# Performance work log

Hardware: AMD Instinct MI355X
Metric: run time of the kernel (lower is better)

## Reference

```python
import jax, jax.numpy as jnp
import numpy as np

B, S, D = 1, 2048, 4096
H, KV, HD = 32, 8, 128
REP = H // KV


def setup_inputs() -> dict:
    key = jax.random.key(0)
    ks = jax.random.split(key, 8)
    x = jax.random.normal(ks[0], (B, S, D), dtype=jnp.float32)
    # RoPE tables: freqs_cis[s, j] = exp(i * s * theta_j), theta_j = 10000^(-2j/HD)
    inv_freq = 1.0 / (10000.0 ** (jnp.arange(0, HD, 2, dtype=jnp.float32) / HD))  # [HD/2]
    ang = jnp.arange(S, dtype=jnp.float32)[:, None] * inv_freq[None, :]          # [S, HD/2]
    freqs_cos, freqs_sin = jnp.cos(ang), jnp.sin(ang)
    # causal additive mask [S, S]
    mask = jnp.where(jnp.tril(jnp.ones((S, S), dtype=bool)), 0.0, -1e9).astype(jnp.float32)
    scale = 0.02
    wq = jax.random.normal(ks[1], (D, H * HD), dtype=jnp.float32) * scale
    wk = jax.random.normal(ks[2], (D, KV * HD), dtype=jnp.float32) * scale
    wv = jax.random.normal(ks[3], (D, KV * HD), dtype=jnp.float32) * scale
    wo = jax.random.normal(ks[4], (H * HD, D), dtype=jnp.float32) * scale
    return {"x": x, "freqs_cos": freqs_cos, "freqs_sin": freqs_sin, "mask": mask,
            "wq": wq, "wk": wk, "wv": wv, "wo": wo, "start_pos": 0}


def _rope(t, cos, sin):
    # t: [B, S, nH, HD]; cos/sin: [S, HD/2]. Complex mult on interleaved pairs.
    b, s, h, hd = t.shape
    tp = t.reshape(b, s, h, hd // 2, 2)
    a, bb = tp[..., 0], tp[..., 1]
    c = cos[None, :, None, :]
    sn = sin[None, :, None, :]
    out = jnp.stack([a * c - bb * sn, a * sn + bb * c], axis=-1)
    return out.reshape(b, s, h, hd)


def reference(x, freqs_cos, freqs_sin, mask, wq, wk, wv, wo, start_pos):
    bsz, seqlen, _ = x.shape
    xq = (x @ wq).reshape(bsz, seqlen, H, HD)
    xk = (x @ wk).reshape(bsz, seqlen, KV, HD)
    xv = (x @ wv).reshape(bsz, seqlen, KV, HD)
    xq = _rope(xq, freqs_cos, freqs_sin)
    xk = _rope(xk, freqs_cos, freqs_sin)
    # start_pos == 0: cache = current xk/xv. GQA: group queries by kv head
    # instead of duplicating K/V (same math as repeat_kv).
    q = xq.reshape(bsz, seqlen, KV, REP, HD)
    scores = jnp.einsum('bqkrd,bskd->bkrqs', q, xk) / np.sqrt(HD).astype(np.float32)
    scores = scores + mask[None, None, None, :, :]
    probs = jax.nn.softmax(scores.astype(jnp.float32), axis=-1).astype(x.dtype)
    out = jnp.einsum('bkrqs,bskd->bqkrd', probs, xv)
    out = out.reshape(bsz, seqlen, H * HD)
    return out @ wo
```

## Files before the change

kernel.cpp:

```cpp
#include <hip/hip_runtime.h>

typedef unsigned short u16;
typedef unsigned int u32;
typedef unsigned long long u64;

typedef float f32x4 __attribute__((ext_vector_type(4)));
typedef __bf16 bf16x8 __attribute__((ext_vector_type(8)));
typedef u16 u16x4 __attribute__((ext_vector_type(4)));
typedef u16 u16x8 __attribute__((ext_vector_type(8)));
typedef float fx4 __attribute__((ext_vector_type(4)));


static __device__ __forceinline__ u16 f2b(float f) {
  u32 u = __builtin_bit_cast(u32, f);
  return (u16)((u + 0x7fffu + ((u >> 16) & 1u)) >> 16);
}
static __device__ __forceinline__ float b2f(u16 b) {
  return __builtin_bit_cast(float, ((u32)b) << 16);
}
static __device__ __forceinline__ void gload_lds16(const void* g, void* l) {
  auto gp = (const __attribute__((address_space(1))) u32*)(u64)g;
  auto lp = (__attribute__((address_space(3))) u32*)(u32)(u64)l;
  __builtin_amdgcn_global_load_lds(gp, lp, 16, 0, 0);
}

__global__ __launch_bounds__(256) void cast_bf16_kernel(const float* __restrict__ in,
                                                        u16* __restrict__ out) {
  size_t i = (size_t)(blockIdx.x * 256 + threadIdx.x) * 4;
  fx4 v = *(const fx4*)(in + i);
  u16x4 o;
  o[0] = f2b(v[0]); o[1] = f2b(v[1]); o[2] = f2b(v[2]); o[3] = f2b(v[3]);
  *(u16x4*)(out + i) = o;
}

__global__ __launch_bounds__(256) void wtrans_kernel(const float* __restrict__ in,
                                                     u16* __restrict__ out, int K, int N) {
  __shared__ float tile[32][33];
  int n0 = blockIdx.x * 32, k0 = blockIdx.y * 32;
  int t = threadIdx.x;
  int r = t >> 3, c4 = (t & 7) * 4;
  fx4 v = *(const fx4*)(in + (size_t)(k0 + r) * N + n0 + c4);
  tile[r][c4 + 0] = v[0]; tile[r][c4 + 1] = v[1];
  tile[r][c4 + 2] = v[2]; tile[r][c4 + 3] = v[3];
  __syncthreads();
  u16x4 o;
  o[0] = f2b(tile[c4 + 0][r]); o[1] = f2b(tile[c4 + 1][r]);
  o[2] = f2b(tile[c4 + 2][r]); o[3] = f2b(tile[c4 + 3][r]);
  *(u16x4*)(out + (size_t)(n0 + r) * K + k0 + c4) = o;
}

template <int NH, int LD>
__global__ __launch_bounds__(256) void rope_kernel(u16* __restrict__ x,
                                                   const float* __restrict__ cosb,
                                                   const float* __restrict__ sinb) {
  int tid = blockIdx.x * 256 + threadIdx.x;
  int s = tid / (NH * 16);
  int rem = tid % (NH * 16);
  int h = rem >> 4, c = rem & 15;
  u16* p = x + (size_t)s * LD + h * 128 + c * 8;
  u16x8 v = *(const u16x8*)p;
  fx4 cs = *(const fx4*)(cosb + s * 64 + c * 4);
  fx4 sn = *(const fx4*)(sinb + s * 64 + c * 4);
  u16x8 o;
#pragma unroll
  for (int j = 0; j < 4; ++j) {
    float a = b2f(v[2 * j]), b = b2f(v[2 * j + 1]);
    o[2 * j]     = f2b(a * cs[j] - b * sn[j]);
    o[2 * j + 1] = f2b(a * sn[j] + b * cs[j]);
  }
  *(u16x8*)p = o;
}

__global__ __launch_bounds__(256) void vtrans_kernel(const u16* __restrict__ vb,
                                                     u16* __restrict__ vT) {
  __shared__ u16 tile[64][72];
  int s0 = blockIdx.x * 64;
  int d0 = blockIdx.y * 64;
  int h  = blockIdx.z;
  int t = threadIdx.x;
#pragma unroll
  for (int it = 0; it < 2; ++it) {
    int lin = it * 2048 + t * 8;
    int r = lin >> 6, c = lin & 63;
    u16x8 v = *(const u16x8*)(vb + (size_t)(s0 + r) * 6144 + h * 128 + d0 + c);
#pragma unroll
    for (int j = 0; j < 8; ++j) tile[r][c + j] = v[j];
  }
  __syncthreads();
#pragma unroll
  for (int it = 0; it < 2; ++it) {
    int lin = it * 2048 + t * 8;
    int dd = lin >> 6, ss = lin & 63;
    u16x8 o;
#pragma unroll
    for (int j = 0; j < 8; ++j) o[j] = tile[ss + j][dd];
    *(u16x8*)(vT + (size_t)h * 262144 + (size_t)(d0 + dd) * 2048 + s0 + ss) = o;
  }
}

template <int OUT_BF16>
__global__ __launch_bounds__(256) void gemm_bt_kernel(const u16* __restrict__ A,
                                                      const u16* __restrict__ Bt,
                                                      void* __restrict__ Cv,
                                                      int M, int N, int K) {
  __shared__ u16 sA[128 * 64];
  __shared__ u16 sB[128 * 64];
  const int tid = threadIdx.x;
  const int lane = tid & 63;
  const int w = tid >> 6;
  const int wr = w >> 1, wc = w & 1;
  const int l15 = lane & 15, l4 = lane >> 4;
  const int cpx = gridDim.x >> 3;
  const int swz = ((int)blockIdx.x & 7) * cpx + ((int)blockIdx.x >> 3);
  const int m0 = (swz & 15) * 128;
  const int n0 = (swz >> 4) * 128;

  f32x4 acc[4][4] = {};

  for (int kt = 0; kt < K; kt += 64) {
#pragma unroll
    for (int it = 0; it < 4; ++it) {
      int off = it * 4096 + tid * 16;
      int row = off >> 7;
      int c = ((off >> 4) & 7) ^ (row & 7);
      gload_lds16(A + (size_t)(m0 + row) * K + kt + c * 8, (char*)sA + off);
      gload_lds16(Bt + (size_t)(n0 + row) * K + kt + c * 8, (char*)sB + off);
    }
    __syncthreads();
#pragma unroll
    for (int ks = 0; ks < 2; ++ks) {
      bf16x8 av[4], bv[4];
#pragma unroll
      for (int i = 0; i < 4; ++i) {
        int arow = wr * 64 + i * 16 + l15;
        av[i] = *(const bf16x8*)((char*)sA + arow * 128 + (((ks * 4 + l4) ^ (arow & 7)) << 4));
        int brow = wc * 64 + i * 16 + l15;
        bv[i] = *(const bf16x8*)((char*)sB + brow * 128 + (((ks * 4 + l4) ^ (brow & 7)) << 4));
      }
#pragma unroll
      for (int i = 0; i < 4; ++i)
#pragma unroll
        for (int j = 0; j < 4; ++j)
          acc[i][j] = __builtin_amdgcn_mfma_f32_16x16x32_bf16(av[i], bv[j], acc[i][j], 0, 0, 0);
    }
    __syncthreads();
  }

#pragma unroll
  for (int i = 0; i < 4; ++i)
#pragma unroll
    for (int j = 0; j < 4; ++j) {
      int col = n0 + wc * 64 + j * 16 + l15;
#pragma unroll
      for (int r = 0; r < 4; ++r) {
        int row = m0 + wr * 64 + i * 16 + l4 * 4 + r;
        if (OUT_BF16) ((u16*)Cv)[(size_t)row * N + col] = f2b(acc[i][j][r]);
        else          ((float*)Cv)[(size_t)row * N + col] = acc[i][j][r];
      }
    }
}

__global__ __launch_bounds__(256) void attn_kernel(const u16* __restrict__ qkv,
                                                   const u16* __restrict__ vT,
                                                   u16* __restrict__ ob) {
  __shared__ u16 sK[2][64 * 128];
  __shared__ u16 sV[2][64 * 128];
  __shared__ u16 sP[4][32 * 64];
  const int tid = threadIdx.x, lane = tid & 63, w = tid >> 6;
  const int l15 = lane & 15, l4 = lane >> 4;
  const int h = blockIdx.x;
  const int t = 15 - (int)blockIdx.y;
  const int kvh = h >> 2;
  const int q0 = t * 128;
  const int nt = 2 * t + 2;
  const float scale = 0.08838834764831845f;

  const u16* qb = qkv;
  const u16* kb = qkv + 4096;

  bf16x8 aq[2][4];
#pragma unroll
  for (int m = 0; m < 2; ++m)
#pragma unroll
    for (int kc = 0; kc < 4; ++kc)
      aq[m][kc] = *(const bf16x8*)(qb + (size_t)(q0 + w * 32 + m * 16 + l15) * 6144 +
                                   h * 128 + kc * 32 + l4 * 8);

  f32x4 o[2][8] = {};
  float mrun[2][4], lrun[2][4];
#pragma unroll
  for (int m = 0; m < 2; ++m)
#pragma unroll
    for (int i = 0; i < 4; ++i) { mrun[m][i] = -1e30f; lrun[m][i] = 0.f; }

  auto STAGE = [&](int b, int tt) {
    int s0 = tt * 64;
#pragma unroll
    for (int it = 0; it < 4; ++it) {
      int off = it * 4096 + tid * 16;
      int row = off >> 8;
      int c = ((off >> 4) & 15) ^ (row & 15);
      gload_lds16(kb + (size_t)(s0 + row) * 6144 + kvh * 128 + c * 8, (char*)sK[b] + off);
    }
#pragma unroll
    for (int it = 0; it < 4; ++it) {
      int off = it * 4096 + tid * 16;
      int row = off >> 7;
      int c = ((off >> 4) & 7) ^ (row & 7);
      gload_lds16(vT + (size_t)kvh * 262144 + (size_t)row * 2048 + s0 + c * 8,
                  (char*)sV[b] + off);
    }
  };

  STAGE(0, 0);
  __syncthreads();
  int cur = 0;

  for (int tt = 0; tt < nt; ++tt) {
    if (tt + 1 < nt) STAGE(cur ^ 1, tt + 1);
    int s0 = tt * 64;
    u16* wp = &sP[w][0];

#pragma unroll
    for (int m = 0; m < 2; ++m) {
      const int frow0 = q0 + w * 32 + m * 16;
      if (s0 > frow0 + 15) continue;
      const bool has_mask = (s0 + 63 > frow0);

      f32x4 sf[4] = {};
#pragma unroll
      for (int kc = 0; kc < 4; ++kc) {
#pragma unroll
        for (int j = 0; j < 4; ++j) {
          int krow = j * 16 + l15;
          bf16x8 bk = *(const bf16x8*)((char*)sK[cur] + krow * 256 +
                                       (((kc * 4 + l4) ^ (krow & 15)) << 4));
          sf[j] = __builtin_amdgcn_mfma_f32_16x16x32_bf16(aq[m][kc], bk, sf[j], 0, 0, 0);
        }
      }

      float pv[4][4], mloc[4], lsum[4];
#pragma unroll
      for (int i = 0; i < 4; ++i) mloc[i] = -1e30f;
#pragma unroll
      for (int j = 0; j < 4; ++j) {
        int col = s0 + j * 16 + l15;
#pragma unroll
        for (int i = 0; i < 4; ++i) {
          float v = sf[j][i] * scale;
          if (has_mask && col > frow0 + l4 * 4 + i) v = -1e9f;
          pv[j][i] = v;
          mloc[i] = fmaxf(mloc[i], v);
        }
      }
#pragma unroll
      for (int off = 1; off < 16; off <<= 1)
#pragma unroll
        for (int i = 0; i < 4; ++i) mloc[i] = fmaxf(mloc[i], __shfl_xor(mloc[i], off, 64));
      float alpha[4];
#pragma unroll
      for (int i = 0; i < 4; ++i) {
        float mn = fmaxf(mrun[m][i], mloc[i]);
        alpha[i] = __expf(mrun[m][i] - mn);
        mrun[m][i] = mn;
        lsum[i] = 0.f;
      }
#pragma unroll
      for (int j = 0; j < 4; ++j)
#pragma unroll
        for (int i = 0; i < 4; ++i) {
          float p = __expf(pv[j][i] - mrun[m][i]);
          pv[j][i] = p;
          lsum[i] += p;
        }
#pragma unroll
      for (int off = 1; off < 16; off <<= 1)
#pragma unroll
        for (int i = 0; i < 4; ++i) lsum[i] += __shfl_xor(lsum[i], off, 64);
#pragma unroll
      for (int i = 0; i < 4; ++i) lrun[m][i] = lrun[m][i] * alpha[i] + lsum[i];
#pragma unroll
      for (int n = 0; n < 8; ++n)
#pragma unroll
        for (int i = 0; i < 4; ++i) o[m][n][i] *= alpha[i];

#pragma unroll
      for (int j = 0; j < 4; ++j)
#pragma unroll
        for (int i = 0; i < 4; ++i) {
          int r = m * 16 + l4 * 4 + i;
          int colb = (j * 16 + l15) * 2;
          *(u16*)((char*)wp + r * 128 + (colb ^ ((r & 7) << 4))) = f2b(pv[j][i]);
        }
#pragma unroll
      for (int ks = 0; ks < 2; ++ks) {
        int prow = m * 16 + l15;
        int pb = (ks * 32 + l4 * 8) * 2;
        bf16x8 pa = *(const bf16x8*)((char*)wp + prow * 128 + (pb ^ ((prow & 7) << 4)));
#pragma unroll
        for (int n = 0; n < 8; ++n) {
          int vrow = n * 16 + l15;
          bf16x8 vv = *(const bf16x8*)((char*)sV[cur] + vrow * 128 +
                                       (((ks * 4 + l4) ^ (vrow & 7)) << 4));
          o[m][n] = __builtin_amdgcn_mfma_f32_16x16x32_bf16(pa, vv, o[m][n], 0, 0, 0);
        }
      }
    }
    __syncthreads();
    cur ^= 1;
  }

#pragma unroll
  for (int m = 0; m < 2; ++m) {
    float rcp[4];
#pragma unroll
    for (int i = 0; i < 4; ++i) rcp[i] = 1.f / lrun[m][i];
#pragma unroll
    for (int n = 0; n < 8; ++n)
#pragma unroll
      for (int i = 0; i < 4; ++i) {
        int row = q0 + w * 32 + m * 16 + l4 * 4 + i;
        int col = h * 128 + n * 16 + l15;
        ob[(size_t)row * 4096 + col] = f2b(o[m][n][i] * rcp[i]);
      }
  }
}

extern "C" void kernel_launch(void* const* d_in, const int* in_sizes, int n_in,
                              void* d_out, int out_size, void* d_ws, size_t ws_size,
                              hipStream_t stream) {
  const float* x  = (const float*)d_in[0];
  const float* fc = (const float*)d_in[1];
  const float* fs = (const float*)d_in[2];
  const float* wq = (const float*)d_in[4];
  const float* wk = (const float*)d_in[5];
  const float* wv = (const float*)d_in[6];
  const float* wo = (const float*)d_in[7];
  float* out = (float*)d_out;
  char* ws = (char*)d_ws;

  u16* xb   = (u16*)(ws + 0);
  u16* qkv  = (u16*)(ws + 16777216);
  u16* ob   = (u16*)(ws + 41943040);
  u16* wT   = (u16*)(ws + 58720256);
  u16* vT   = (u16*)(ws + 109051904);
  u16* woT  = wT;

  cast_bf16_kernel<<<8192, 256, 0, stream>>>(x, xb);
  wtrans_kernel<<<dim3(128, 128), 256, 0, stream>>>(wq, wT, 4096, 4096);
  wtrans_kernel<<<dim3(32, 128), 256, 0, stream>>>(wk, wT + (size_t)4096 * 4096, 4096, 1024);
  wtrans_kernel<<<dim3(32, 128), 256, 0, stream>>>(wv, wT + (size_t)5120 * 4096, 4096, 1024);

  gemm_bt_kernel<1><<<768, 256, 0, stream>>>(xb, wT, qkv, 2048, 6144, 4096);

  rope_kernel<32, 6144><<<4096, 256, 0, stream>>>(qkv, fc, fs);
  rope_kernel<8, 6144><<<1024, 256, 0, stream>>>(qkv + 4096, fc, fs);
  vtrans_kernel<<<dim3(32, 2, 8), 256, 0, stream>>>(qkv + 5120, vT);

  attn_kernel<<<dim3(32, 16), 256, 0, stream>>>(qkv, vT, ob);

  wtrans_kernel<<<dim3(128, 128), 256, 0, stream>>>(wo, woT, 4096, 4096);
  gemm_bt_kernel<0><<<512, 256, 0, stream>>>(ob, woT, out, 2048, 4096, 4096);
}
```

Before: 550.2 us.

## Replace GEMM with 8-wave 128x256 tile double-buffered pipelined kernel

Swaps the 4-wave 128x128 GEMM for an 8-wave kernel that computes 128x256 output tiles. It double-buffers K/2 half-stages in LDS and overlaps async global-to-LDS loads with MFMA work, using explicit vmcnt waits, barriers and setprio. The goal is to hide global-load latency and get more reuse per tile for both the QKV and output projections. In exchange it raises LDS use, allows one block per CU, and halves the number of blocks. It also makes a trivial hoist of the mask row base in attention.

```diff
diff --git a/kernel.cpp b/kernel.cpp
--- a/kernel.cpp
+++ b/kernel.cpp
@@ -98,64 +98,110 @@
   }
 }
 
+#define SWA(r, c) (((r) >> 1) * 128 + ((((r) & 1) * 4 + ((c) ^ (((r) >> 1) & 3))) << 4))
 template <int OUT_BF16>
-__global__ __launch_bounds__(256) void gemm_bt_kernel(const u16* __restrict__ A,
-                                                      const u16* __restrict__ Bt,
-                                                      void* __restrict__ Cv,
-                                                      int M, int N, int K) {
-  __shared__ u16 sA[128 * 64];
-  __shared__ u16 sB[128 * 64];
+__global__ __launch_bounds__(512, 1) void gemm8_kernel(const u16* __restrict__ A,
+                                                       const u16* __restrict__ Bt,
+                                                       void* __restrict__ Cv,
+                                                       int M, int N, int K) {
+  __shared__ u16 sA[2][2][4096];
+  __shared__ u16 sB[2][2][8192];
   const int tid = threadIdx.x;
   const int lane = tid & 63;
   const int w = tid >> 6;
-  const int wr = w >> 1, wc = w & 1;
+  const int wm = w >> 2, wn = w & 3;
   const int l15 = lane & 15, l4 = lane >> 4;
   const int cpx = gridDim.x >> 3;
   const int swz = ((int)blockIdx.x & 7) * cpx + ((int)blockIdx.x >> 3);
   const int m0 = (swz & 15) * 128;
-  const int n0 = (swz >> 4) * 128;
+  const int n0 = (swz >> 4) * 256;
 
   f32x4 acc[4][4] = {};
 
-  for (int kt = 0; kt < K; kt += 64) {
-#pragma unroll
-    for (int it = 0; it < 4; ++it) {
-      int off = it * 4096 + tid * 16;
-      int row = off >> 7;
-      int c = ((off >> 4) & 7) ^ (row & 7);
-      gload_lds16(A + (size_t)(m0 + row) * K + kt + c * 8, (char*)sA + off);
-      gload_lds16(Bt + (size_t)(n0 + row) * K + kt + c * 8, (char*)sB + off);
-    }
-    __syncthreads();
-#pragma unroll
-    for (int ks = 0; ks < 2; ++ks) {
-      bf16x8 av[4], bv[4];
-#pragma unroll
-      for (int i = 0; i < 4; ++i) {
-        int arow = wr * 64 + i * 16 + l15;
-        av[i] = *(const bf16x8*)((char*)sA + arow * 128 + (((ks * 4 + l4) ^ (arow & 7)) << 4));
-        int brow = wc * 64 + i * 16 + l15;
-        bv[i] = *(const bf16x8*)((char*)sB + brow * 128 + (((ks * 4 + l4) ^ (brow & 7)) << 4));
-      }
-#pragma unroll
-      for (int i = 0; i < 4; ++i)
-#pragma unroll
-        for (int j = 0; j < 4; ++j)
-          acc[i][j] = __builtin_amdgcn_mfma_f32_16x16x32_bf16(av[i], bv[j], acc[i][j], 0, 0, 0);
-    }
-    __syncthreads();
-  }
-
-#pragma unroll
-  for (int i = 0; i < 4; ++i)
-#pragma unroll
-    for (int j = 0; j < 4; ++j) {
-      int col = n0 + wc * 64 + j * 16 + l15;
+  auto STAGE = [&](int stT, int stKh) {
+    int sd = stT & 1;
+    {
+      int off = tid * 16;
+      int L = off >> 7, s = (off >> 4) & 7;
+      int r = 2 * L + (s >> 2), c = (s & 3) ^ (L & 3);
+      gload_lds16(A + (size_t)(m0 + r) * K + stT * 64 + stKh * 32 + c * 8,
+                  (char*)&sA[sd][stKh][0] + off);
+    }
+#pragma unroll
+    for (int u = 0; u < 2; ++u) {
+      int off = tid * 16 + u * 8192;
+      int L = off >> 7, s = (off >> 4) & 7;
+      int r = 2 * L + (s >> 2), c = (s & 3) ^ (L & 3);
+      gload_lds16(Bt + (size_t)(n0 + r) * K + stT * 64 + stKh * 32 + c * 8,
+                  (char*)&sB[sd][stKh][0] + off);
+    }
+  };
+
+  auto PHASE = [&](int d, int kh, int stT, int stKh, bool doStage) {
+    const char* aB = (const char*)&sA[d][kh][0];
+    const char* bB = (const char*)&sB[d][kh][0];
+    bf16x8 av[4], bv[4];
+#pragma unroll
+    for (int f = 0; f < 4; ++f) {
+      av[f] = *(const bf16x8*)(aB + SWA(wm * 64 + f * 16 + l15, l4));
+      bv[f] = *(const bf16x8*)(bB + SWA(wn * 64 + f * 16 + l15, l4));
+    }
+    if (doStage) STAGE(stT, stKh);
+    __builtin_amdgcn_s_barrier();
+    asm volatile("s_waitcnt lgkmcnt(0)" ::: "memory");
+    __builtin_amdgcn_sched_barrier(0);
+    __builtin_amdgcn_s_setprio(1);
+#pragma unroll
+    for (int fi = 0; fi < 4; ++fi)
+#pragma unroll
+      for (int fj = 0; fj < 4; ++fj)
+        acc[fi][fj] = __builtin_amdgcn_mfma_f32_16x16x32_bf16(av[fi], bv[fj], acc[fi][fj], 0, 0, 0);
+    __builtin_amdgcn_s_setprio(0);
+    __builtin_amdgcn_sched_barrier(0);
+  };
+
+  const int nt = K >> 6;
+  STAGE(0, 0);
+  STAGE(0, 1);
+  STAGE(1, 0);
+  asm volatile("s_waitcnt vmcnt(6)" ::: "memory");
+  __builtin_amdgcn_s_barrier();
+
+  for (int t = 0; t < nt - 2; ++t) {
+    PHASE(t & 1, 0, t + 1, 1, true);
+    asm volatile("s_waitcnt vmcnt(6)" ::: "memory");
+    __builtin_amdgcn_s_barrier();
+    PHASE(t & 1, 1, t + 2, 0, true);
+    asm volatile("s_waitcnt vmcnt(6)" ::: "memory");
+    __builtin_amdgcn_s_barrier();
+  }
+  {
+    int t = nt - 2;
+    PHASE(t & 1, 0, t + 1, 1, true);
+    asm volatile("s_waitcnt vmcnt(6)" ::: "memory");
+    __builtin_amdgcn_s_barrier();
+    PHASE(t & 1, 1, 0, 0, false);
+    asm volatile("s_waitcnt vmcnt(3)" ::: "memory");
+    __builtin_amdgcn_s_barrier();
+  }
+  {
+    int t = nt - 1;
+    PHASE(t & 1, 0, 0, 0, false);
+    asm volatile("s_waitcnt vmcnt(0)" ::: "memory");
+    __builtin_amdgcn_s_barrier();
+    PHASE(t & 1, 1, 0, 0, false);
+  }
+
+#pragma unroll
+  for (int fi = 0; fi < 4; ++fi)
+#pragma unroll
+    for (int fj = 0; fj < 4; ++fj) {
+      int col = n0 + wn * 64 + fj * 16 + l15;
 #pragma unroll
       for (int r = 0; r < 4; ++r) {
-        int row = m0 + wr * 64 + i * 16 + l4 * 4 + r;
-        if (OUT_BF16) ((u16*)Cv)[(size_t)row * N + col] = f2b(acc[i][j][r]);
-        else          ((float*)Cv)[(size_t)row * N + col] = acc[i][j][r];
+        int row = m0 + wm * 64 + fi * 16 + l4 * 4 + r;
+        if (OUT_BF16) ((u16*)Cv)[(size_t)row * N + col] = f2b(acc[fi][fj][r]);
+        else          ((float*)Cv)[(size_t)row * N + col] = acc[fi][fj][r];
       }
     }
 }
@@ -239,6 +285,7 @@
         }
       }
 
+      const int qrow_base = frow0 + l4 * 4;
       float pv[4][4], mloc[4], lsum[4];
 #pragma unroll
       for (int i = 0; i < 4; ++i) mloc[i] = -1e30f;
@@ -248,7 +295,7 @@
 #pragma unroll
         for (int i = 0; i < 4; ++i) {
           float v = sf[j][i] * scale;
-          if (has_mask && col > frow0 + l4 * 4 + i) v = -1e9f;
+          if (has_mask && col > qrow_base + i) v = -1e9f;
           pv[j][i] = v;
           mloc[i] = fmaxf(mloc[i], v);
         }
@@ -351,7 +398,7 @@
   wtrans_kernel<<<dim3(32, 128), 256, 0, stream>>>(wk, wT + (size_t)4096 * 4096, 4096, 1024);
   wtrans_kernel<<<dim3(32, 128), 256, 0, stream>>>(wv, wT + (size_t)5120 * 4096, 4096, 1024);
 
-  gemm_bt_kernel<1><<<768, 256, 0, stream>>>(xb, wT, qkv, 2048, 6144, 4096);
+  gemm8_kernel<1><<<384, 512, 0, stream>>>(xb, wT, qkv, 2048, 6144, 4096);
 
   rope_kernel<32, 6144><<<4096, 256, 0, stream>>>(qkv, fc, fs);
   rope_kernel<8, 6144><<<1024, 256, 0, stream>>>(qkv + 4096, fc, fs);
@@ -360,5 +407,5 @@
   attn_kernel<<<dim3(32, 16), 256, 0, stream>>>(qkv, vT, ob);
 
   wtrans_kernel<<<dim3(128, 128), 256, 0, stream>>>(wo, woT, 4096, 4096);
-  gemm_bt_kernel<0><<<512, 256, 0, stream>>>(ob, woT, out, 2048, 4096, 4096);
-}
+  gemm8_kernel<0><<<256, 512, 0, stream>>>(ob, woT, out, 2048, 4096, 4096);
+}
```

New measurement: 567.8 us. 3.2% more time.

## Transpose attention MFMA operands so each lane owns one query row

Applied to the files above, without the earlier changes.

Swaps the A/B operands of both MFMAs in the attention kernel so score and output tiles are transposed, with each lane holding a single query row. The softmax max and sum reductions drop from four-step 16-lane shuffles on four values to two cross-group shuffles on one value. Running max and sum shrink to scalars per m. P stores and output stores become packed 4-wide writes. The P scratch buffer is halved. The risk is a different LDS bank-conflict pattern on the P writes and the strided output stores.

```diff
diff --git a/kernel.cpp b/kernel.cpp
--- a/kernel.cpp
+++ b/kernel.cpp
@@ -165,7 +165,7 @@
                                                    u16* __restrict__ ob) {
   __shared__ u16 sK[2][64 * 128];
   __shared__ u16 sV[2][64 * 128];
-  __shared__ u16 sP[4][32 * 64];
+  __shared__ u16 sP[4][16 * 64];
   const int tid = threadIdx.x, lane = tid & 63, w = tid >> 6;
   const int l15 = lane & 15, l4 = lane >> 4;
   const int h = blockIdx.x;
@@ -187,11 +187,9 @@
                                    h * 128 + kc * 32 + l4 * 8);
 
   f32x4 o[2][8] = {};
-  float mrun[2][4], lrun[2][4];
-#pragma unroll
-  for (int m = 0; m < 2; ++m)
-#pragma unroll
-    for (int i = 0; i < 4; ++i) { mrun[m][i] = -1e30f; lrun[m][i] = 0.f; }
+  float mrun[2], lrun[2];
+#pragma unroll
+  for (int m = 0; m < 2; ++m) { mrun[m] = -1e30f; lrun[m] = 0.f; }
 
   auto STAGE = [&](int b, int tt) {
     int s0 = tt * 64;
@@ -226,6 +224,7 @@
       const int frow0 = q0 + w * 32 + m * 16;
       if (s0 > frow0 + 15) continue;
       const bool has_mask = (s0 + 63 > frow0);
+      const int q_abs = frow0 + l15;
 
       f32x4 sf[4] = {};
 #pragma unroll
@@ -235,74 +234,62 @@
           int krow = j * 16 + l15;
           bf16x8 bk = *(const bf16x8*)((char*)sK[cur] + krow * 256 +
                                        (((kc * 4 + l4) ^ (krow & 15)) << 4));
-          sf[j] = __builtin_amdgcn_mfma_f32_16x16x32_bf16(aq[m][kc], bk, sf[j], 0, 0, 0);
+          sf[j] = __builtin_amdgcn_mfma_f32_16x16x32_bf16(bk, aq[m][kc], sf[j], 0, 0, 0);
         }
       }
 
-      float pv[4][4], mloc[4], lsum[4];
-#pragma unroll
-      for (int i = 0; i < 4; ++i) mloc[i] = -1e30f;
-#pragma unroll
-      for (int j = 0; j < 4; ++j) {
-        int col = s0 + j * 16 + l15;
+      float pv16[4][4];
+      float pmax = -1e30f;
+#pragma unroll
+      for (int j = 0; j < 4; ++j)
 #pragma unroll
         for (int i = 0; i < 4; ++i) {
           float v = sf[j][i] * scale;
-          if (has_mask && col > frow0 + l4 * 4 + i) v = -1e9f;
-          pv[j][i] = v;
-          mloc[i] = fmaxf(mloc[i], v);
+          if (has_mask && (s0 + 16 * j + 4 * l4 + i) > q_abs) v = -1e9f;
+          pv16[j][i] = v;
+          pmax = fmaxf(pmax, v);
         }
-      }
-#pragma unroll
-      for (int off = 1; off < 16; off <<= 1)
-#pragma unroll
-        for (int i = 0; i < 4; ++i) mloc[i] = fmaxf(mloc[i], __shfl_xor(mloc[i], off, 64));
-      float alpha[4];
-#pragma unroll
-      for (int i = 0; i < 4; ++i) {
-        float mn = fmaxf(mrun[m][i], mloc[i]);
-        alpha[i] = __expf(mrun[m][i] - mn);
-        mrun[m][i] = mn;
-        lsum[i] = 0.f;
-      }
+      pmax = fmaxf(pmax, __shfl_xor(pmax, 16, 64));
+      pmax = fmaxf(pmax, __shfl_xor(pmax, 32, 64));
+      float mn = fmaxf(mrun[m], pmax);
+      float alpha = __expf(mrun[m] - mn);
+      mrun[m] = mn;
+      float psum = 0.f;
 #pragma unroll
       for (int j = 0; j < 4; ++j)
 #pragma unroll
         for (int i = 0; i < 4; ++i) {
-          float p = __expf(pv[j][i] - mrun[m][i]);
-          pv[j][i] = p;
-          lsum[i] += p;
+          float p = __expf(pv16[j][i] - mn);
+          pv16[j][i] = p;
+          psum += p;
         }
-#pragma unroll
-      for (int off = 1; off < 16; off <<= 1)
-#pragma unroll
-        for (int i = 0; i < 4; ++i) lsum[i] += __shfl_xor(lsum[i], off, 64);
-#pragma unroll
-      for (int i = 0; i < 4; ++i) lrun[m][i] = lrun[m][i] * alpha[i] + lsum[i];
+      psum += __shfl_xor(psum, 16, 64);
+      psum += __shfl_xor(psum, 32, 64);
+      lrun[m] = lrun[m] * alpha + psum;
 #pragma unroll
       for (int n = 0; n < 8; ++n)
 #pragma unroll
-        for (int i = 0; i < 4; ++i) o[m][n][i] *= alpha[i];
-
-#pragma unroll
-      for (int j = 0; j < 4; ++j)
-#pragma unroll
-        for (int i = 0; i < 4; ++i) {
-          int r = m * 16 + l4 * 4 + i;
-          int colb = (j * 16 + l15) * 2;
-          *(u16*)((char*)wp + r * 128 + (colb ^ ((r & 7) << 4))) = f2b(pv[j][i]);
-        }
+        for (int r = 0; r < 4; ++r) o[m][n][r] *= alpha;
+
+#pragma unroll
+      for (int j = 0; j < 4; ++j) {
+        u16x4 pk;
+#pragma unroll
+        for (int i = 0; i < 4; ++i) pk[i] = f2b(pv16[j][i]);
+        int colb = (16 * j + 4 * l4) * 2;
+        *(u16x4*)((char*)wp + l15 * 128 + (colb ^ ((l15 & 7) << 4))) = pk;
+      }
+
 #pragma unroll
       for (int ks = 0; ks < 2; ++ks) {
-        int prow = m * 16 + l15;
-        int pb = (ks * 32 + l4 * 8) * 2;
-        bf16x8 pa = *(const bf16x8*)((char*)wp + prow * 128 + (pb ^ ((prow & 7) << 4)));
+        int pcb = (ks * 32 + l4 * 8) * 2;
+        bf16x8 pb = *(const bf16x8*)((char*)wp + l15 * 128 + (pcb ^ ((l15 & 7) << 4)));
 #pragma unroll
         for (int n = 0; n < 8; ++n) {
           int vrow = n * 16 + l15;
           bf16x8 vv = *(const bf16x8*)((char*)sV[cur] + vrow * 128 +
                                        (((ks * 4 + l4) ^ (vrow & 7)) << 4));
-          o[m][n] = __builtin_amdgcn_mfma_f32_16x16x32_bf16(pa, vv, o[m][n], 0, 0, 0);
+          o[m][n] = __builtin_amdgcn_mfma_f32_16x16x32_bf16(vv, pb, o[m][n], 0, 0, 0);
         }
       }
     }
@@ -312,17 +299,15 @@
 
 #pragma unroll
   for (int m = 0; m < 2; ++m) {
-    float rcp[4];
-#pragma unroll
-    for (int i = 0; i < 4; ++i) rcp[i] = 1.f / lrun[m][i];
-#pragma unroll
-    for (int n = 0; n < 8; ++n)
-#pragma unroll
-      for (int i = 0; i < 4; ++i) {
-        int row = q0 + w * 32 + m * 16 + l4 * 4 + i;
-        int col = h * 128 + n * 16 + l15;
-        ob[(size_t)row * 4096 + col] = f2b(o[m][n][i] * rcp[i]);
-      }
+    float rcp = 1.f / lrun[m];
+    size_t qrow = (size_t)(q0 + w * 32 + m * 16 + l15);
+#pragma unroll
+    for (int n = 0; n < 8; ++n) {
+      u16x4 pk;
+#pragma unroll
+      for (int r = 0; r < 4; ++r) pk[r] = f2b(o[m][n][r] * rcp);
+      *(u16x4*)(ob + qrow * 4096 + h * 128 + n * 16 + l4 * 4) = pk;
+    }
   }
 }
 
```

After: 533.6 us. 3.0% less time.
